# Optimization experiments

Measured on AMD Instinct MI355X. Metric: run time of the kernel, lower is better.

The kernel has to match this reference:

```python
import jax, jax.numpy as jnp
import numpy as np


def conv2d(x, w, b, pad):
    # NCHW / OIHW conv, stride 1
    y = jax.lax.conv_general_dilated(x, w, (1, 1), [(pad, pad), (pad, pad)],
                                     dimension_numbers=('NCHW', 'OIHW', 'NCHW'))
    return y + b[None, :, None, None]


def deform_conv2d(x, offset, modulator, w_reg, b_reg):
    # Faithful reimplementation of torchvision.ops.deform_conv2d (stride=1,
    # pad=K//2, dilation=1, 1 offset group), offset layout [B, 2*K*K, H, W]
    # with (dy, dx) pairs per kernel tap.
    B, C, H, W = x.shape
    K = w_reg.shape[-1]
    KK = K * K
    pad = K // 2
    off = offset.reshape(B, KK, 2, H, W)
    ks_y = (jnp.arange(KK) // K - pad).astype(x.dtype)
    ks_x = (jnp.arange(KK) % K - pad).astype(x.dtype)
    hh = jnp.arange(H, dtype=x.dtype)
    ww = jnp.arange(W, dtype=x.dtype)
    # sampling coords per (batch, kernel tap, out_y, out_x)
    py = hh[None, None, :, None] + ks_y[None, :, None, None] + off[:, :, 0]
    px = ww[None, None, None, :] + ks_x[None, :, None, None] + off[:, :, 1]
    y0 = jnp.floor(py)
    x0 = jnp.floor(px)
    ly = py - y0
    lx = px - x0
    y0i = y0.astype(jnp.int32)
    x0i = x0.astype(jnp.int32)
    x_flat = x.reshape(B, C, H * W)

    def gather(yi, xi, wgt):
        valid = (yi >= 0) & (yi < H) & (xi >= 0) & (xi < W)
        idx = (jnp.clip(yi, 0, H - 1) * W + jnp.clip(xi, 0, W - 1)).reshape(B, KK, H * W)
        v = jnp.take_along_axis(x_flat[:, :, None, :], idx[:, None], axis=3)  # [B,C,KK,HW]
        w = (wgt * valid.astype(x.dtype)).reshape(B, 1, KK, H * W)
        return v * w

    v = (gather(y0i, x0i, (1 - ly) * (1 - lx))
         + gather(y0i, x0i + 1, (1 - ly) * lx)
         + gather(y0i + 1, x0i, ly * (1 - lx))
         + gather(y0i + 1, x0i + 1, ly * lx))
    v = v * modulator.reshape(B, 1, KK, H * W)
    out = jnp.einsum('bckn,ock->bon', v, w_reg.reshape(w_reg.shape[0], C, KK))
    return out.reshape(B, -1, H, W) + b_reg[None, :, None, None]


def setup_inputs() -> dict:
    key = jax.random.key(0)
    ks = jax.random.split(key, 14)
    B, C, H, W = 8, 256, 64, 64
    K = 3
    Cr = C // 4  # SE ratio=4
    x = jax.random.normal(ks[0], (B, C, H, W), jnp.float32)
    # small offset-conv weights keep sampled offsets modest (torchvision inits these to 0)
    w_off = jax.random.normal(ks[1], (2 * K * K, C, K, K), jnp.float32) * 0.01
    b_off = jax.random.normal(ks[2], (2 * K * K,), jnp.float32) * 0.01
    w_mod = jax.random.normal(ks[3], (K * K, C, K, K), jnp.float32) * 0.01
    b_mod = jax.random.normal(ks[4], (K * K,), jnp.float32) * 0.01
    w_reg = jax.random.normal(ks[5], (C, C, K, K), jnp.float32) * (1.0 / np.sqrt(C * K * K))
    b_reg = jax.random.normal(ks[6], (C,), jnp.float32) * 0.01
    w_se1 = jax.random.normal(ks[7], (Cr, C), jnp.float32) * (1.0 / np.sqrt(C))
    b_se1 = jnp.zeros((Cr,), jnp.float32)
    w_se2 = jax.random.normal(ks[8], (C, Cr), jnp.float32) * (1.0 / np.sqrt(Cr))
    b_se2 = jnp.zeros((C,), jnp.float32)
    w_mask = jax.random.normal(ks[9], (C, C, 1, 1), jnp.float32) * (1.0 / np.sqrt(C))
    b_mask = jnp.zeros((C,), jnp.float32)
    return {"x": x, "w_off": w_off, "b_off": b_off, "w_mod": w_mod, "b_mod": b_mod,
            "w_reg": w_reg, "b_reg": b_reg, "w_se1": w_se1, "b_se1": b_se1,
            "w_se2": w_se2, "b_se2": b_se2, "w_mask": w_mask, "b_mask": b_mask}


def reference(x, w_off, b_off, w_mod, b_mod, w_reg, b_reg,
              w_se1, b_se1, w_se2, b_se2, w_mask, b_mask):
    # DeformableConv2d
    offset = conv2d(x, w_off, b_off, pad=1)
    modulator = 2.0 * jax.nn.sigmoid(conv2d(x, w_mod, b_mod, pad=1))
    f = deform_conv2d(x, offset, modulator, w_reg, b_reg)
    # SEBlock('avg', ch, ratio=4)
    s = jnp.mean(f, axis=(2, 3))                       # [B, C]
    s = jax.nn.relu(s @ w_se1.T + b_se1)               # [B, C/4]
    s = jax.nn.sigmoid(s @ w_se2.T + b_se2)            # [B, C]
    f = f * s[:, :, None, None]
    # mask = Hardsigmoid(Conv1x1(x))
    m = conv2d(x, w_mask, b_mask, pad=0)
    m = jnp.clip(m / 6.0 + 0.5, 0.0, 1.0)
    return f * m + x
```

## Files before the change

kernel.cpp:

```cpp
#include <hip/hip_runtime.h>
#include <math.h>

#define HWSZ 4096
#define C_ 256
#define B_ 8

#define M_WS      0
#define XB_WS     4194304
#define WT2_WS    8388608
#define SMEAN_WS  8753152
#define SSCALE_WS 8755200

typedef __attribute__((ext_vector_type(8))) short short8;
typedef __attribute__((ext_vector_type(4))) float f32x4;

__device__ __forceinline__ uint bfr(float a) {
  uint u = __float_as_uint(a);
  return (u + 0x7fffu + ((u >> 16) & 1u)) >> 16;
}
__device__ __forceinline__ uint pk2(float a, float b) { return bfr(a) | (bfr(b) << 16); }
__device__ __forceinline__ float bff(ushort u) { return __uint_as_float((uint)u << 16); }
__device__ __forceinline__ float lo16(uint u) { return __uint_as_float(u << 16); }
__device__ __forceinline__ float hi16(uint u) { return __uint_as_float(u & 0xffff0000u); }

__global__ __launch_bounds__(256) void k0_weights(
    const float* __restrict__ w_reg, const float* __restrict__ w_mask,
    const float* __restrict__ w_off, const float* __restrict__ w_mod,
    float* __restrict__ ws) {
  int i = blockIdx.x * 256 + threadIdx.x;
  const int nwt = 10 * 65536;
  const int total = nwt + 9 * 32 * 256;
  if (i >= total) {
    int z = i - total;
    if (z < 2048) ws[SMEAN_WS + z] = 0.f;
    return;
  }
  float v;
  if (i < 9 * 65536) {
    int kk = i >> 16, o = (i >> 8) & 255, c = i & 255;
    v = w_reg[(o * C_ + c) * 9 + kk];
  } else if (i < nwt) {
    v = w_mask[i - 9 * 65536];
  } else {
    int e = i - nwt;
    int s = e >> 13, r = e & 8191;
    int o2 = r >> 8, c = r & 255;
    if (o2 < 18)      v = w_off[(o2 * C_ + c) * 9 + s];
    else if (o2 < 27) v = w_mod[((o2 - 18) * C_ + c) * 9 + s];
    else              v = 0.f;
  }
  ((ushort*)(ws + WT2_WS))[i] = (ushort)bfr(v);
}

__global__ __launch_bounds__(256) void k0b_nhwc(const float* __restrict__ x,
                                                float* __restrict__ ws) {
  __shared__ float tile[64][65];
  int b = blockIdx.x >> 6, hw0 = (blockIdx.x & 63) << 6;
  int t = threadIdx.x;
  uint* xb = (uint*)(ws + XB_WS) + ((size_t)b << 19);
  int rr = t >> 6, cc = t & 63;
  int e = t & 7, hwp = t >> 3;
  for (int cg = 0; cg < 4; cg++) {
    __syncthreads();
    const float* xp = x + ((size_t)(b * 256 + cg * 64 + rr)) * HWSZ + hw0 + cc;
    #pragma unroll
    for (int r0 = 0; r0 < 64; r0 += 4)
      tile[r0 + rr][cc] = xp[(size_t)r0 * HWSZ];
    __syncthreads();
    #pragma unroll
    for (int h2 = 0; h2 < 2; h2++) {
      int hw_l = h2 * 32 + hwp;
      int c2 = e * 8;
      uint4 val;
      val.x = pk2(tile[c2][hw_l], tile[c2 + 1][hw_l]);
      val.y = pk2(tile[c2 + 2][hw_l], tile[c2 + 3][hw_l]);
      val.z = pk2(tile[c2 + 4][hw_l], tile[c2 + 5][hw_l]);
      val.w = pk2(tile[c2 + 6][hw_l], tile[c2 + 7][hw_l]);
      *(uint4*)&xb[(size_t)(hw0 + hw_l) * 128 + cg * 32 + e * 4] = val;
    }
  }
}

__global__ __launch_bounds__(512, 4) void k2_fused(
    const float* __restrict__ b_off, const float* __restrict__ b_mod,
    const float* __restrict__ b_reg, const float* __restrict__ b_mask,
    float* __restrict__ ws, float* __restrict__ out) {
  __shared__ uint vb[2][64 * 128];
  __shared__ float offmod[27 * 64];

  int bl = ((blockIdx.x & 7) << 6) | (blockIdx.x >> 3);
  int b = bl >> 6, h = bl & 63;
  int t = threadIdx.x;
  int lane = t & 63, w = t >> 6;
  const int hwid = t >> 5;
  const int cl = lane & 31;
  const ushort* xb2 = (const ushort*)(ws + XB_WS) + ((size_t)b << 20);
  const ushort* wt2 = (const ushort*)(ws + WT2_WS);
  const ushort* wom = wt2 + 10 * 65536;
  const int fr = lane & 15, fq = lane >> 4;

  auto widx = [&](int n) -> uint {
    return (uint)n * 128u + (((uint)cl * 4u) ^ ((uint)(n & 7) << 2));
  };
  auto makeRecs = [&](int kk, int nl, float* wg, int* ix) {
    float dy = offmod[(2 * kk) * 64 + nl];
    float dx = offmod[(2 * kk + 1) * 64 + nl];
    float md = offmod[(18 + kk) * 64 + nl];
    float py = (float)(h + kk / 3 - 1) + dy;
    float px = (float)(nl + kk % 3 - 1) + dx;
    float fy = floorf(py), fx = floorf(px);
    float ly = py - fy, lx = px - fx;
    int y0 = (int)fy, x0 = (int)fx;
    int y1 = y0 + 1, x1 = x0 + 1;
    float vy0 = ((unsigned)y0 < 64u) ? 1.f : 0.f;
    float vy1 = ((unsigned)y1 < 64u) ? 1.f : 0.f;
    float vx0 = ((unsigned)x0 < 64u) ? 1.f : 0.f;
    float vx1 = ((unsigned)x1 < 64u) ? 1.f : 0.f;
    int cy0 = min(max(y0, 0), 63), cy1 = min(max(y1, 0), 63);
    int cx0 = min(max(x0, 0), 63), cx1 = min(max(x1, 0), 63);
    ix[0] = cy0 * 64 + cx0; wg[0] = (1.f - ly) * (1.f - lx) * md * vy0 * vx0;
    ix[1] = cy0 * 64 + cx1; wg[1] = (1.f - ly) * lx * md * vy0 * vx1;
    ix[2] = cy1 * 64 + cx0; wg[2] = ly * (1.f - lx) * md * vy1 * vx0;
    ix[3] = cy1 * 64 + cx1; wg[3] = ly * lx * md * vy1 * vx1;
  };
  auto gatherTap = [&](int kk, uint buf) {
    #pragma unroll
    for (int p = 0; p < 4; p++) {
      int n = p * 16 + hwid;
      float wg[4]; int ix[4];
      makeRecs(kk, n, wg, ix);
      float a0 = 0.f, a1 = 0.f, a2 = 0.f, a3 = 0.f, a4 = 0.f, a5 = 0.f, a6 = 0.f, a7 = 0.f;
      #pragma unroll
      for (int cr = 0; cr < 4; cr++) {
        uint4 dd = *(const uint4*)(xb2 + (size_t)ix[cr] * 256 + cl * 8);
        float wv = wg[cr];
        a0 = fmaf(wv, lo16(dd.x), a0); a1 = fmaf(wv, hi16(dd.x), a1);
        a2 = fmaf(wv, lo16(dd.y), a2); a3 = fmaf(wv, hi16(dd.y), a3);
        a4 = fmaf(wv, lo16(dd.z), a4); a5 = fmaf(wv, hi16(dd.z), a5);
        a6 = fmaf(wv, lo16(dd.w), a6); a7 = fmaf(wv, hi16(dd.w), a7);
      }
      *(uint4*)&vb[buf][widx(n)] =
          make_uint4(pk2(a0, a1), pk2(a2, a3), pk2(a4, a5), pk2(a6, a7));
    }
  };
  auto gatherShift = [&](int s, uint buf) {
    int row = h + s / 3 - 1;
    #pragma unroll
    for (int p = 0; p < 4; p++) {
      int n = p * 16 + hwid;
      int col = n + s % 3 - 1;
      uint4 v = make_uint4(0, 0, 0, 0);
      if (((unsigned)row < 64u) && ((unsigned)col < 64u))
        v = *(const uint4*)(xb2 + ((size_t)(row * 64 + col)) * 256 + cl * 8);
      *(uint4*)&vb[buf][widx(n)] = v;
    }
  };
  auto gatherMask = [&](uint buf) {
    #pragma unroll
    for (int p = 0; p < 4; p++) {
      int n = p * 16 + hwid;
      uint4 v = *(const uint4*)(xb2 + ((size_t)(h * 64 + n)) * 256 + cl * 8);
      *(uint4*)&vb[buf][widx(n)] = v;
    }
  };

  f32x4 aom = (f32x4)0.f;
  const int m0 = w >> 2, nt0 = w & 3;
  gatherShift(0, 0);
  __syncthreads();
  for (int s = 0; s < 9; s++) {
    const uint cur = s & 1;
    const ushort* wp = wom + (size_t)s * 8192;
    for (int ks = 0; ks < 8; ks++) {
      short8 af = *(const short8*)(wp + (m0 * 16 + fr) * 256 + ks * 32 + fq * 8);
      int bn = nt0 * 16 + fr;
      uint idx = (uint)bn * 128u + (((uint)(ks * 16 + fq * 4)) ^ ((uint)(bn & 7) << 2));
      short8 bf = *(const short8*)&vb[cur][idx];
      aom = __builtin_amdgcn_mfma_f32_16x16x32_bf16(af, bf, aom, 0, 0, 0);
    }
    if (s < 8) gatherShift(s + 1, cur ^ 1);
    __syncthreads();
  }
  #pragma unroll
  for (int r = 0; r < 4; r++) {
    int o = m0 * 16 + fq * 4 + r;
    int nn = nt0 * 16 + fr;
    if (o < 18) {
      offmod[o * 64 + nn] = aom[r] + b_off[o];
    } else if (o < 27) {
      float v = aom[r] + b_mod[o - 18];
      offmod[o * 64 + nn] = 2.f / (1.f + expf(-v));
    }
  }
  __syncthreads();

  f32x4 acc[2][4];
  #pragma unroll
  for (int mt = 0; mt < 2; mt++)
    #pragma unroll
    for (int nt = 0; nt < 4; nt++) acc[mt][nt] = (f32x4)0.f;
  const int o0 = w << 5;
  float* sme = ws + SMEAN_WS + b * 256;
  ushort* mws = (ushort*)(ws + M_WS);

  gatherTap(0, 0);
  __syncthreads();

  for (int kk = 0; kk < 10; kk++) {
    const uint cur = kk & 1;
    const ushort* wtap = wt2 + (size_t)kk * 65536;
    for (int ks = 0; ks < 8; ks++) {
      short8 af0 = *(const short8*)(wtap + (o0 + fr) * 256 + ks * 32 + fq * 8);
      short8 af1 = *(const short8*)(wtap + (o0 + 16 + fr) * 256 + ks * 32 + fq * 8);
      #pragma unroll
      for (int nt = 0; nt < 4; nt++) {
        int bn = nt * 16 + fr;
        uint idx = (uint)bn * 128u + (((uint)(ks * 16 + fq * 4)) ^ ((uint)(bn & 7) << 2));
        short8 bf = *(const short8*)&vb[cur][idx];
        acc[0][nt] = __builtin_amdgcn_mfma_f32_16x16x32_bf16(af0, bf, acc[0][nt], 0, 0, 0);
        acc[1][nt] = __builtin_amdgcn_mfma_f32_16x16x32_bf16(af1, bf, acc[1][nt], 0, 0, 0);
      }
    }
    if (kk == 8) {
      #pragma unroll
      for (int mt = 0; mt < 2; mt++)
        #pragma unroll
        for (int r = 0; r < 4; r++) {
          int o = o0 + mt * 16 + fq * 4 + r;
          float bo = b_reg[o];
          float* op = out + (size_t)(b * C_ + o) * HWSZ + h * 64;
          float so = 0.f;
          #pragma unroll
          for (int nt = 0; nt < 4; nt++) {
            float fv = acc[mt][nt][r] + bo;
            op[nt * 16 + fr] = fv;
            so += fv;
            acc[mt][nt][r] = 0.f;
          }
          so += __shfl_xor(so, 1);
          so += __shfl_xor(so, 2);
          so += __shfl_xor(so, 4);
          so += __shfl_xor(so, 8);
          if (fr == 0) atomicAdd(&sme[o], so);
        }
    }
    if (kk < 8)       gatherTap(kk + 1, cur ^ 1);
    else if (kk == 8) gatherMask(cur ^ 1);
    if (kk < 9) __syncthreads();
  }

  #pragma unroll
  for (int mt = 0; mt < 2; mt++)
    #pragma unroll
    for (int r = 0; r < 4; r++) {
      int o = o0 + mt * 16 + fq * 4 + r;
      float bm = b_mask[o];
      ushort* mp = mws + (size_t)(b * C_ + o) * HWSZ + h * 64;
      #pragma unroll
      for (int nt = 0; nt < 4; nt++) {
        float mv = fminf(fmaxf((acc[mt][nt][r] + bm) * (1.f / 6.f) + 0.5f, 0.f), 1.f);
        mp[nt * 16 + fr] = (ushort)bfr(mv);
      }
    }
}

__global__ __launch_bounds__(256) void k4_se(
    const float* __restrict__ w_se1, const float* __restrict__ b_se1,
    const float* __restrict__ w_se2, const float* __restrict__ b_se2,
    float* __restrict__ ws) {
  __shared__ float sm[2048];
  __shared__ float s1[512];
  int t = threadIdx.x;
  for (int e = t; e < 2048; e += 256) sm[e] = ws[SMEAN_WS + e] * (1.f / HWSZ);
  __syncthreads();
  for (int e = t; e < 512; e += 256) {
    int b = e >> 6, cr = e & 63;
    float a = b_se1[cr];
    for (int c = 0; c < 256; c++) a += sm[b * 256 + c] * w_se1[cr * 256 + c];
    s1[e] = fmaxf(a, 0.f);
  }
  __syncthreads();
  for (int e = t; e < 2048; e += 256) {
    int b = e >> 8, c = e & 255;
    float a = b_se2[c];
    for (int cr = 0; cr < 64; cr++) a += s1[b * 64 + cr] * w_se2[c * 64 + cr];
    ws[SSCALE_WS + e] = 1.f / (1.f + expf(-a));
  }
}

__global__ __launch_bounds__(256) void k5_final(const float* __restrict__ x,
                                                const float* __restrict__ ws,
                                                float* __restrict__ out) {
  const ushort* mws = (const ushort*)(ws + M_WS);
  int i4 = blockIdx.x * 256 + threadIdx.x;
  const int total = B_ * C_ * HWSZ / 4;
  for (; i4 < total; i4 += gridDim.x * 256) {
    int i = i4 * 4;
    int bc = i >> 12;
    float s = ws[SSCALE_WS + bc];
    float4 f = *(const float4*)&out[i];
    uint2 mu = *(const uint2*)&mws[i];
    float4 xv = *(const float4*)&x[i];
    float4 r;
    r.x = f.x * s * bff((ushort)(mu.x & 0xffffu)) + xv.x;
    r.y = f.y * s * bff((ushort)(mu.x >> 16)) + xv.y;
    r.z = f.z * s * bff((ushort)(mu.y & 0xffffu)) + xv.z;
    r.w = f.w * s * bff((ushort)(mu.y >> 16)) + xv.w;
    *(float4*)&out[i] = r;
  }
}

extern "C" void kernel_launch(void* const* d_in, const int* in_sizes, int n_in,
                              void* d_out, int out_size, void* d_ws, size_t ws_size,
                              hipStream_t stream) {
  const float* x      = (const float*)d_in[0];
  const float* w_off  = (const float*)d_in[1];
  const float* b_off  = (const float*)d_in[2];
  const float* w_mod  = (const float*)d_in[3];
  const float* b_mod  = (const float*)d_in[4];
  const float* w_reg  = (const float*)d_in[5];
  const float* b_reg  = (const float*)d_in[6];
  const float* w_se1  = (const float*)d_in[7];
  const float* b_se1  = (const float*)d_in[8];
  const float* w_se2  = (const float*)d_in[9];
  const float* b_se2  = (const float*)d_in[10];
  const float* w_mask = (const float*)d_in[11];
  const float* b_mask = (const float*)d_in[12];
  float* out = (float*)d_out;
  float* ws  = (float*)d_ws;

  k0_weights<<<dim3(2856), dim3(256), 0, stream>>>(w_reg, w_mask, w_off, w_mod, ws);
  k0b_nhwc<<<dim3(512), dim3(256), 0, stream>>>(x, ws);
  k2_fused<<<dim3(512), dim3(512), 0, stream>>>(b_off, b_mod, b_reg, b_mask, ws, out);
  k4_se<<<dim3(1), dim3(256), 0, stream>>>(w_se1, b_se1, w_se2, b_se2, ws);
  k5_final<<<dim3(2048), dim3(256), 0, stream>>>(x, ws, out);
}
```

Before: 210.4 us.

## Stage padded input rows once for offset conv, fuse mask GEMM, parallelize SE

The offset/modulator 3x3 conv now stages each of the three input rows once, as a 66-column padded tile, and reads shifted column windows from it. Before, nine shifted copies were gathered. The 1x1 mask GEMM is folded into the middle-row stage and its result written early, which shortens the main tap loop to nine iterations. Offsets and modulators are packed as float4 records for a single LDS read, and s_setprio wraps the MFMA loops. The SE kernel is split across 8 blocks, one per batch, instead of a single block. The cost is slightly more LDS and extra register pressure, since mask accumulators share the accumulators that are reset afterwards.

```diff
diff --git a/kernel.cpp b/kernel.cpp
--- a/kernel.cpp
+++ b/kernel.cpp
@@ -85,8 +85,8 @@
     const float* __restrict__ b_off, const float* __restrict__ b_mod,
     const float* __restrict__ b_reg, const float* __restrict__ b_mask,
     float* __restrict__ ws, float* __restrict__ out) {
-  __shared__ uint vb[2][64 * 128];
-  __shared__ float offmod[27 * 64];
+  __shared__ uint vbraw[2][66 * 128];
+  __shared__ float omrf[9 * 64 * 4];
 
   int bl = ((blockIdx.x & 7) << 6) | (blockIdx.x >> 3);
   int b = bl >> 6, h = bl & 63;
@@ -99,13 +99,32 @@
   const ushort* wom = wt2 + 10 * 65536;
   const int fr = lane & 15, fq = lane >> 4;
 
-  auto widx = [&](int n) -> uint {
-    return (uint)n * 128u + (((uint)cl * 4u) ^ ((uint)(n & 7) << 2));
+  auto widxP = [&](int pcol) -> uint {
+    return (uint)pcol * 128u + (((uint)cl * 4u) ^ ((uint)(pcol & 7) << 2));
+  };
+  auto stageRow = [&](int row, int buf) {
+    bool rv = ((unsigned)row < 64u);
+    #pragma unroll
+    for (int p = 0; p < 4; p++) {
+      int pcol = p * 16 + hwid;
+      int col = pcol - 1;
+      uint4 v = make_uint4(0, 0, 0, 0);
+      if (rv && ((unsigned)col < 64u))
+        v = *(const uint4*)(xb2 + ((size_t)(row * 64 + col)) * 256 + cl * 8);
+      *(uint4*)&vbraw[buf][widxP(pcol)] = v;
+    }
+    if (hwid < 2) {
+      int pcol = 64 + hwid;
+      int col = pcol - 1;
+      uint4 v = make_uint4(0, 0, 0, 0);
+      if (rv && col < 64)
+        v = *(const uint4*)(xb2 + ((size_t)(row * 64 + col)) * 256 + cl * 8);
+      *(uint4*)&vbraw[buf][widxP(pcol)] = v;
+    }
   };
   auto makeRecs = [&](int kk, int nl, float* wg, int* ix) {
-    float dy = offmod[(2 * kk) * 64 + nl];
-    float dx = offmod[(2 * kk + 1) * 64 + nl];
-    float md = offmod[(18 + kk) * 64 + nl];
+    const float4 rec = *(const float4*)&omrf[kk * 256 + nl * 4];
+    float dy = rec.x, dx = rec.y, md = rec.z;
     float py = (float)(h + kk / 3 - 1) + dy;
     float px = (float)(nl + kk % 3 - 1) + dx;
     float fy = floorf(py), fx = floorf(px);
@@ -123,7 +142,7 @@
     ix[2] = cy1 * 64 + cx0; wg[2] = ly * (1.f - lx) * md * vy1 * vx0;
     ix[3] = cy1 * 64 + cx1; wg[3] = ly * lx * md * vy1 * vx1;
   };
-  auto gatherTap = [&](int kk, uint buf) {
+  auto gatherTap = [&](int kk, int buf) {
     #pragma unroll
     for (int p = 0; p < 4; p++) {
       int n = p * 16 + hwid;
@@ -139,114 +158,113 @@
         a4 = fmaf(wv, lo16(dd.z), a4); a5 = fmaf(wv, hi16(dd.z), a5);
         a6 = fmaf(wv, lo16(dd.w), a6); a7 = fmaf(wv, hi16(dd.w), a7);
       }
-      *(uint4*)&vb[buf][widx(n)] =
+      *(uint4*)&vbraw[buf][widxP(n)] =
           make_uint4(pk2(a0, a1), pk2(a2, a3), pk2(a4, a5), pk2(a6, a7));
-    }
-  };
-  auto gatherShift = [&](int s, uint buf) {
-    int row = h + s / 3 - 1;
-    #pragma unroll
-    for (int p = 0; p < 4; p++) {
-      int n = p * 16 + hwid;
-      int col = n + s % 3 - 1;
-      uint4 v = make_uint4(0, 0, 0, 0);
-      if (((unsigned)row < 64u) && ((unsigned)col < 64u))
-        v = *(const uint4*)(xb2 + ((size_t)(row * 64 + col)) * 256 + cl * 8);
-      *(uint4*)&vb[buf][widx(n)] = v;
-    }
-  };
-  auto gatherMask = [&](uint buf) {
-    #pragma unroll
-    for (int p = 0; p < 4; p++) {
-      int n = p * 16 + hwid;
-      uint4 v = *(const uint4*)(xb2 + ((size_t)(h * 64 + n)) * 256 + cl * 8);
-      *(uint4*)&vb[buf][widx(n)] = v;
     }
   };
 
   f32x4 aom = (f32x4)0.f;
   const int m0 = w >> 2, nt0 = w & 3;
-  gatherShift(0, 0);
-  __syncthreads();
-  for (int s = 0; s < 9; s++) {
-    const uint cur = s & 1;
-    const ushort* wp = wom + (size_t)s * 8192;
-    for (int ks = 0; ks < 8; ks++) {
-      short8 af = *(const short8*)(wp + (m0 * 16 + fr) * 256 + ks * 32 + fq * 8);
-      int bn = nt0 * 16 + fr;
-      uint idx = (uint)bn * 128u + (((uint)(ks * 16 + fq * 4)) ^ ((uint)(bn & 7) << 2));
-      short8 bf = *(const short8*)&vb[cur][idx];
-      aom = __builtin_amdgcn_mfma_f32_16x16x32_bf16(af, bf, aom, 0, 0, 0);
-    }
-    if (s < 8) gatherShift(s + 1, cur ^ 1);
-    __syncthreads();
-  }
-  #pragma unroll
-  for (int r = 0; r < 4; r++) {
-    int o = m0 * 16 + fq * 4 + r;
-    int nn = nt0 * 16 + fr;
-    if (o < 18) {
-      offmod[o * 64 + nn] = aom[r] + b_off[o];
-    } else if (o < 27) {
-      float v = aom[r] + b_mod[o - 18];
-      offmod[o * 64 + nn] = 2.f / (1.f + expf(-v));
-    }
-  }
-  __syncthreads();
-
+  const int o0 = w << 5;
   f32x4 acc[2][4];
   #pragma unroll
   for (int mt = 0; mt < 2; mt++)
     #pragma unroll
     for (int nt = 0; nt < 4; nt++) acc[mt][nt] = (f32x4)0.f;
-  const int o0 = w << 5;
+  ushort* mws = (ushort*)(ws + M_WS);
   float* sme = ws + SMEAN_WS + b * 256;
-  ushort* mws = (ushort*)(ws + M_WS);
-
-  gatherTap(0, 0);
+
+  stageRow(h - 1, 0);
   __syncthreads();
-
-  for (int kk = 0; kk < 10; kk++) {
-    const uint cur = kk & 1;
-    const ushort* wtap = wt2 + (size_t)kk * 65536;
-    for (int ks = 0; ks < 8; ks++) {
-      short8 af0 = *(const short8*)(wtap + (o0 + fr) * 256 + ks * 32 + fq * 8);
-      short8 af1 = *(const short8*)(wtap + (o0 + 16 + fr) * 256 + ks * 32 + fq * 8);
-      #pragma unroll
-      for (int nt = 0; nt < 4; nt++) {
-        int bn = nt * 16 + fr;
-        uint idx = (uint)bn * 128u + (((uint)(ks * 16 + fq * 4)) ^ ((uint)(bn & 7) << 2));
-        short8 bf = *(const short8*)&vb[cur][idx];
-        acc[0][nt] = __builtin_amdgcn_mfma_f32_16x16x32_bf16(af0, bf, acc[0][nt], 0, 0, 0);
-        acc[1][nt] = __builtin_amdgcn_mfma_f32_16x16x32_bf16(af1, bf, acc[1][nt], 0, 0, 0);
-      }
-    }
-    if (kk == 8) {
+  for (int e = 0; e < 3; e++) {
+    const int buf = (e == 1) ? 1 : 0;
+    {
+      const int bnA = nt0 * 16 + fr;
+      #pragma unroll
+      for (int s3 = 0; s3 < 3; s3++) {
+        int s = e * 3 + s3;
+        const ushort* wp = wom + (size_t)s * 8192;
+        int pcol = bnA + s3;
+        for (int ks = 0; ks < 8; ks++) {
+          short8 af = *(const short8*)(wp + (m0 * 16 + fr) * 256 + ks * 32 + fq * 8);
+          uint idx = (uint)pcol * 128u + (((uint)(ks * 16 + fq * 4)) ^ ((uint)(pcol & 7) << 2));
+          short8 bf = *(const short8*)&vbraw[buf][idx];
+          aom = __builtin_amdgcn_mfma_f32_16x16x32_bf16(af, bf, aom, 0, 0, 0);
+        }
+      }
+    }
+    if (e == 1) {
+      const ushort* wt9 = wt2 + (size_t)9 * 65536;
+      __builtin_amdgcn_s_setprio(1);
+      for (int ks = 0; ks < 8; ks++) {
+        short8 af0 = *(const short8*)(wt9 + (o0 + fr) * 256 + ks * 32 + fq * 8);
+        short8 af1 = *(const short8*)(wt9 + (o0 + 16 + fr) * 256 + ks * 32 + fq * 8);
+        #pragma unroll
+        for (int nt = 0; nt < 4; nt++) {
+          int pcol = nt * 16 + fr + 1;
+          uint idx = (uint)pcol * 128u + (((uint)(ks * 16 + fq * 4)) ^ ((uint)(pcol & 7) << 2));
+          short8 bf = *(const short8*)&vbraw[1][idx];
+          acc[0][nt] = __builtin_amdgcn_mfma_f32_16x16x32_bf16(af0, bf, acc[0][nt], 0, 0, 0);
+          acc[1][nt] = __builtin_amdgcn_mfma_f32_16x16x32_bf16(af1, bf, acc[1][nt], 0, 0, 0);
+        }
+      }
+      __builtin_amdgcn_s_setprio(0);
+    }
+    if (e == 0)      stageRow(h, 1);
+    else if (e == 1) stageRow(h + 1, 0);
+    else {
       #pragma unroll
       for (int mt = 0; mt < 2; mt++)
         #pragma unroll
         for (int r = 0; r < 4; r++) {
           int o = o0 + mt * 16 + fq * 4 + r;
-          float bo = b_reg[o];
-          float* op = out + (size_t)(b * C_ + o) * HWSZ + h * 64;
-          float so = 0.f;
+          float bm = b_mask[o];
+          ushort* mp = mws + (size_t)(b * C_ + o) * HWSZ + h * 64;
           #pragma unroll
           for (int nt = 0; nt < 4; nt++) {
-            float fv = acc[mt][nt][r] + bo;
-            op[nt * 16 + fr] = fv;
-            so += fv;
+            float mv = fminf(fmaxf((acc[mt][nt][r] + bm) * (1.f / 6.f) + 0.5f, 0.f), 1.f);
+            mp[nt * 16 + fr] = (ushort)bfr(mv);
             acc[mt][nt][r] = 0.f;
           }
-          so += __shfl_xor(so, 1);
-          so += __shfl_xor(so, 2);
-          so += __shfl_xor(so, 4);
-          so += __shfl_xor(so, 8);
-          if (fr == 0) atomicAdd(&sme[o], so);
         }
-    }
-    if (kk < 8)       gatherTap(kk + 1, cur ^ 1);
-    else if (kk == 8) gatherMask(cur ^ 1);
-    if (kk < 9) __syncthreads();
+      #pragma unroll
+      for (int r = 0; r < 4; r++) {
+        int o = m0 * 16 + fq * 4 + r;
+        int nn = nt0 * 16 + fr;
+        if (o < 18) {
+          omrf[(o >> 1) * 256 + nn * 4 + (o & 1)] = aom[r] + b_off[o];
+        } else if (o < 27) {
+          float v = aom[r] + b_mod[o - 18];
+          omrf[(o - 18) * 256 + nn * 4 + 2] = 2.f / (1.f + expf(-v));
+        }
+      }
+    }
+    __syncthreads();
+  }
+
+  gatherTap(0, 1);
+  __syncthreads();
+  for (int kk = 0; kk < 9; kk++) {
+    const int cur = (kk & 1) ^ 1;
+    const ushort* wtap = wt2 + (size_t)kk * 65536;
+    __builtin_amdgcn_s_setprio(1);
+    for (int ks = 0; ks < 8; ks++) {
+      short8 af0 = *(const short8*)(wtap + (o0 + fr) * 256 + ks * 32 + fq * 8);
+      short8 af1 = *(const short8*)(wtap + (o0 + 16 + fr) * 256 + ks * 32 + fq * 8);
+      #pragma unroll
+      for (int nt = 0; nt < 4; nt++) {
+        int bn = nt * 16 + fr;
+        uint idx = (uint)bn * 128u + (((uint)(ks * 16 + fq * 4)) ^ ((uint)(bn & 7) << 2));
+        short8 bf = *(const short8*)&vbraw[cur][idx];
+        acc[0][nt] = __builtin_amdgcn_mfma_f32_16x16x32_bf16(af0, bf, acc[0][nt], 0, 0, 0);
+        acc[1][nt] = __builtin_amdgcn_mfma_f32_16x16x32_bf16(af1, bf, acc[1][nt], 0, 0, 0);
+      }
+    }
+    __builtin_amdgcn_s_setprio(0);
+    if (kk < 8) {
+      gatherTap(kk + 1, cur ^ 1);
+      __syncthreads();
+    }
   }
 
   #pragma unroll
@@ -254,13 +272,20 @@
     #pragma unroll
     for (int r = 0; r < 4; r++) {
       int o = o0 + mt * 16 + fq * 4 + r;
-      float bm = b_mask[o];
-      ushort* mp = mws + (size_t)(b * C_ + o) * HWSZ + h * 64;
+      float bo = b_reg[o];
+      float* op = out + (size_t)(b * C_ + o) * HWSZ + h * 64;
+      float so = 0.f;
       #pragma unroll
       for (int nt = 0; nt < 4; nt++) {
-        float mv = fminf(fmaxf((acc[mt][nt][r] + bm) * (1.f / 6.f) + 0.5f, 0.f), 1.f);
-        mp[nt * 16 + fr] = (ushort)bfr(mv);
-      }
+        float fv = acc[mt][nt][r] + bo;
+        op[nt * 16 + fr] = fv;
+        so += fv;
+      }
+      so += __shfl_xor(so, 1);
+      so += __shfl_xor(so, 2);
+      so += __shfl_xor(so, 4);
+      so += __shfl_xor(so, 8);
+      if (fr == 0) atomicAdd(&sme[o], so);
     }
 }
 
@@ -268,23 +293,22 @@
     const float* __restrict__ w_se1, const float* __restrict__ b_se1,
     const float* __restrict__ w_se2, const float* __restrict__ b_se2,
     float* __restrict__ ws) {
-  __shared__ float sm[2048];
-  __shared__ float s1[512];
+  __shared__ float sm[256];
+  __shared__ float s1[64];
+  int b = blockIdx.x;
   int t = threadIdx.x;
-  for (int e = t; e < 2048; e += 256) sm[e] = ws[SMEAN_WS + e] * (1.f / HWSZ);
+  sm[t] = ws[SMEAN_WS + b * 256 + t] * (1.f / HWSZ);
   __syncthreads();
-  for (int e = t; e < 512; e += 256) {
-    int b = e >> 6, cr = e & 63;
-    float a = b_se1[cr];
-    for (int c = 0; c < 256; c++) a += sm[b * 256 + c] * w_se1[cr * 256 + c];
-    s1[e] = fmaxf(a, 0.f);
+  if (t < 64) {
+    float a = b_se1[t];
+    for (int c = 0; c < 256; c++) a += sm[c] * w_se1[t * 256 + c];
+    s1[t] = fmaxf(a, 0.f);
   }
   __syncthreads();
-  for (int e = t; e < 2048; e += 256) {
-    int b = e >> 8, c = e & 255;
-    float a = b_se2[c];
-    for (int cr = 0; cr < 64; cr++) a += s1[b * 64 + cr] * w_se2[c * 64 + cr];
-    ws[SSCALE_WS + e] = 1.f / (1.f + expf(-a));
+  {
+    float a = b_se2[t];
+    for (int cr = 0; cr < 64; cr++) a += s1[cr] * w_se2[t * 64 + cr];
+    ws[SSCALE_WS + b * 256 + t] = 1.f / (1.f + expf(-a));
   }
 }
 
@@ -332,6 +356,6 @@
   k0_weights<<<dim3(2856), dim3(256), 0, stream>>>(w_reg, w_mask, w_off, w_mod, ws);
   k0b_nhwc<<<dim3(512), dim3(256), 0, stream>>>(x, ws);
   k2_fused<<<dim3(512), dim3(512), 0, stream>>>(b_off, b_mod, b_reg, b_mask, ws, out);
-  k4_se<<<dim3(1), dim3(256), 0, stream>>>(w_se1, b_se1, w_se2, b_se2, ws);
+  k4_se<<<dim3(8), dim3(256), 0, stream>>>(w_se1, b_se1, w_se2, b_se2, ws);
   k5_final<<<dim3(2048), dim3(256), 0, stream>>>(x, ws, out);
 }
```

After: 194.8 us. 1.08x faster.
